# Optimization experiments

Hardware: AMD Instinct MI355X
Metric: run time of the kernel (lower is better)

## Reference

```python
import jax, jax.numpy as jnp
import numpy as np

B, N, D, H, L = 2, 2048, 512, 8, 2
HD = D // H


def setup_inputs() -> dict:
    key = jax.random.key(0)
    ks = jax.random.split(key, 8)
    s = 0.02
    return {
        "inputs_embeds": jax.random.normal(ks[0], (B, N, D), jnp.float32),
        "pos_emb": jax.random.normal(ks[1], (N, D), jnp.float32) * s,
        "c_attn_w": jax.random.normal(ks[2], (L, D, 3 * D), jnp.float32) * s,
        "c_attn_b": jnp.zeros((L, 3 * D), jnp.float32),
        "out_w": jax.random.normal(ks[3], (L, D, D), jnp.float32) * s,
        "out_b": jnp.zeros((L, D), jnp.float32),
        "ln1_g": jnp.ones((L, D), jnp.float32),
        "ln1_b": jnp.zeros((L, D), jnp.float32),
        "c_fc_w": jax.random.normal(ks[4], (L, D, 4 * D), jnp.float32) * s,
        "c_fc_b": jnp.zeros((L, 4 * D), jnp.float32),
        "c_proj_w": jax.random.normal(ks[5], (L, 4 * D, D), jnp.float32) * s,
        "c_proj_b": jnp.zeros((L, D), jnp.float32),
        "ln2_g": jnp.ones((L, D), jnp.float32),
        "ln2_b": jnp.zeros((L, D), jnp.float32),
    }


def _layernorm(x, g, b, eps=1e-5):
    mu = jnp.mean(x, axis=-1, keepdims=True)
    var = jnp.mean(jnp.square(x - mu), axis=-1, keepdims=True)
    return (x - mu) * jax.lax.rsqrt(var + eps) * g + b


def _gelu_new(x):
    # NewGELUActivation: tanh approximation
    return 0.5 * x * (1.0 + jnp.tanh(jnp.sqrt(2.0 / jnp.pi) * (x + 0.044715 * x ** 3)))


def _attention(x, w_qkv, b_qkv, w_out, b_out, self_mask):
    qkv = x @ w_qkv + b_qkv                      # [B,N,3D]
    q, k, v = jnp.split(qkv, 3, axis=-1)
    def heads(t):
        return t.reshape(B, N, H, HD).transpose(0, 2, 1, 3)  # [B,H,N,HD]
    q, k, v = heads(q), heads(k), heads(v)
    scores = jnp.einsum('bhqd,bhkd->bhqk', q, k) / jnp.sqrt(jnp.float32(HD))
    neg = jnp.finfo(scores.dtype).min
    scores = jnp.where(self_mask, scores, neg)   # exclude-self mask
    attn = jax.nn.softmax(scores, axis=-1)
    o = jnp.einsum('bhqk,bhkd->bhqd', attn, v)
    o = o.transpose(0, 2, 1, 3).reshape(B, N, D)
    return o @ w_out + b_out


def reference(inputs_embeds, pos_emb, c_attn_w, c_attn_b, out_w, out_b,
              ln1_g, ln1_b, c_fc_w, c_fc_b, c_proj_w, c_proj_b, ln2_g, ln2_b):
    self_mask = ~jnp.eye(N, dtype=bool)[None, None]  # [1,1,N,N]
    h = inputs_embeds + pos_emb[None]
    for l in range(L):
        res = h
        x = _layernorm(h, ln1_g[l], ln1_b[l])
        h = _attention(x, c_attn_w[l], c_attn_b[l], out_w[l], out_b[l], self_mask) + res
        res = h
        x = _layernorm(h, ln2_g[l], ln2_b[l])
        x = _gelu_new(x @ c_fc_w[l] + c_fc_b[l])
        h = (x @ c_proj_w[l] + c_proj_b[l]) + res
    return h
```

## Files before the change

kernel.cpp:

```cpp
#include <hip/hip_runtime.h>
#include <hip/hip_bf16.h>
#include <math.h>

#define BB 2
#define NN 2048
#define DD 512
#define HH 8
#define LL 2
#define TT (BB*NN)

typedef short short8 __attribute__((ext_vector_type(8)));
typedef float floatx4 __attribute__((ext_vector_type(4)));

__device__ __forceinline__ unsigned short f2b(float v) {
    union { float f; unsigned u; } x; x.f = v;
    unsigned r = x.u + 0x7fff + ((x.u >> 16) & 1);
    return (unsigned short)(r >> 16);
}

__global__ __launch_bounds__(256) void k_bias_add(const float* __restrict__ src,
                                                  const float* __restrict__ bias,
                                                  float* __restrict__ dst) {
    int i = blockIdx.x * 256 + threadIdx.x;
    dst[i] = src[i] + bias[i & (DD - 1)];
}

template <int EMB>
__global__ __launch_bounds__(256) void k_ln(const float* __restrict__ hin,
                                            unsigned short* __restrict__ xout,
                                            const float* __restrict__ g,
                                            const float* __restrict__ b,
                                            const float* __restrict__ emb,
                                            const float* __restrict__ pos,
                                            float* __restrict__ hout) {
    __shared__ float red[4];
    __shared__ float bc1, bc2;
    int t = blockIdx.x;
    int tid = threadIdx.x;
    int lane = tid & 63, wv = tid >> 6;
    float v0, v1;
    if (EMB) {
        const float* erow = emb + (size_t)t * DD;
        const float* prow = pos + (size_t)(t & (NN - 1)) * DD;
        v0 = erow[tid] + prow[tid];
        v1 = erow[tid + 256] + prow[tid + 256];
        hout[(size_t)t * DD + tid] = v0;
        hout[(size_t)t * DD + tid + 256] = v1;
    } else {
        const float* row = hin + (size_t)t * DD;
        v0 = row[tid];
        v1 = row[tid + 256];
    }

    float s = v0 + v1;
#pragma unroll
    for (int o = 32; o; o >>= 1) s += __shfl_down(s, o, 64);
    if (lane == 0) red[wv] = s;
    __syncthreads();
    if (tid == 0) bc1 = (red[0] + red[1] + red[2] + red[3]) * (1.0f / DD);
    __syncthreads();
    float mu = bc1;
    float d0 = v0 - mu, d1 = v1 - mu;
    s = d0 * d0 + d1 * d1;
#pragma unroll
    for (int o = 32; o; o >>= 1) s += __shfl_down(s, o, 64);
    if (lane == 0) red[wv] = s;
    __syncthreads();
    if (tid == 0) bc2 = (red[0] + red[1] + red[2] + red[3]) * (1.0f / DD);
    __syncthreads();
    float rstd = rsqrtf(bc2 + 1e-5f);
    xout[(size_t)t * DD + tid]       = f2b(d0 * rstd * g[tid] + b[tid]);
    xout[(size_t)t * DD + tid + 256] = f2b(d1 * rstd * g[tid + 256] + b[tid + 256]);
}

__device__ __forceinline__ float gelu_new(float v) {
    const float c = 0.7978845608028654f;
    float u = c * (v + 0.044715f * v * v * v);
    return 0.5f * v * (1.0f + tanhf(u));
}

#define PL 3145728
__global__ __launch_bounds__(256) void k_wt_all(const float* __restrict__ c_attn_w,
                                                const float* __restrict__ out_w,
                                                const float* __restrict__ c_fc_w,
                                                const float* __restrict__ c_proj_w,
                                                unsigned short* __restrict__ wbuf) {
    __shared__ unsigned short t[64][72];
    int bx = blockIdx.x;
    int l = bx / 768;
    int r = bx - l * 768;
    const float* W; unsigned short* WT; int K, N;
    if (r < 192)      { W = c_attn_w + (size_t)l * 512 * 1536; WT = wbuf + (size_t)l * PL;           K = 512;  N = 1536; }
    else if (r < 256) { r -= 192; W = out_w  + (size_t)l * 512 * 512;  WT = wbuf + (size_t)l * PL + 786432;  K = 512;  N = 512; }
    else if (r < 512) { r -= 256; W = c_fc_w + (size_t)l * 512 * 2048; WT = wbuf + (size_t)l * PL + 1048576; K = 512;  N = 2048; }
    else              { r -= 512; W = c_proj_w + (size_t)l * 2048 * 512; WT = wbuf + (size_t)l * PL + 2097152; K = 2048; N = 512; }
    int tiles_n = N >> 6;
    int n0 = (r % tiles_n) * 64, k0 = (r / tiles_n) * 64;

    int tid = threadIdx.x;
    int rr = tid >> 2;
    int c0 = (tid & 3) * 16;
    const float* src = W + (size_t)(k0 + rr) * N + n0 + c0;
#pragma unroll
    for (int u = 0; u < 4; u++) {
        float4 v = *(const float4*)&src[u * 4];
        t[c0 + u * 4 + 0][rr] = f2b(v.x);
        t[c0 + u * 4 + 1][rr] = f2b(v.y);
        t[c0 + u * 4 + 2][rr] = f2b(v.z);
        t[c0 + u * 4 + 3][rr] = f2b(v.w);
    }
    __syncthreads();
    unsigned short* dst = WT + (size_t)(n0 + rr) * K + k0 + c0;
#pragma unroll
    for (int u = 0; u < 4; u++)
        *(uint2*)&dst[u * 4] = *(const uint2*)&t[rr][c0 + u * 4];
}

template <int ACT, int BF16OUT, int ATOMIC>
__global__ __launch_bounds__(256) void k_mgemm(const unsigned short* __restrict__ Ab,
                                               const unsigned short* __restrict__ Bt,
                                               const float* __restrict__ bias,
                                               float* __restrict__ Cp,
                                               unsigned short* __restrict__ Cb,
                                               int Kfull, int Kchunk, int N) {
    __shared__ unsigned short Als[2][8 * 512];
    __shared__ unsigned short Bls[2][8 * 512];

    int tid = threadIdx.x;
    int l = tid & 63, w = tid >> 6;
    int wm = w >> 1, wn = w & 1;
    int m0 = blockIdx.y * 128, n0 = blockIdx.x * 128;
    int kb = blockIdx.z * Kchunk;
    int lr = l & 15;
    int lk = (l >> 4) * 8;

    const unsigned short* Ap0 = Ab + (size_t)(m0 + (w * 2 + 0) * 16 + lr) * Kfull + kb + lk;
    const unsigned short* Ap1 = Ab + (size_t)(m0 + (w * 2 + 1) * 16 + lr) * Kfull + kb + lk;
    const unsigned short* Bp0 = Bt + (size_t)(n0 + (w * 2 + 0) * 16 + lr) * Kfull + kb + lk;
    const unsigned short* Bp1 = Bt + (size_t)(n0 + (w * 2 + 1) * 16 + lr) * Kfull + kb + lk;
    int la0 = (w * 2 + 0) * 512 + l * 8;
    int la1 = (w * 2 + 1) * 512 + l * 8;

    floatx4 acc[4][4];
#pragma unroll
    for (int i = 0; i < 4; i++)
#pragma unroll
        for (int j = 0; j < 4; j++) acc[i][j] = (floatx4){0.f, 0.f, 0.f, 0.f};

    int nit = Kchunk >> 5;

    uint4 ra0 = *(const uint4*)Ap0;
    uint4 ra1 = *(const uint4*)Ap1;
    uint4 rb0 = *(const uint4*)Bp0;
    uint4 rb1 = *(const uint4*)Bp1;
    *(uint4*)&Als[0][la0] = ra0;
    *(uint4*)&Als[0][la1] = ra1;
    *(uint4*)&Bls[0][la0] = rb0;
    *(uint4*)&Bls[0][la1] = rb1;
    if (nit > 1) {
        ra0 = *(const uint4*)(Ap0 + 32);
        ra1 = *(const uint4*)(Ap1 + 32);
        rb0 = *(const uint4*)(Bp0 + 32);
        rb1 = *(const uint4*)(Bp1 + 32);
    }
    __syncthreads();

    for (int it = 0; it < nit; it++) {
        int c = it & 1;
        if (it + 1 < nit) {
            *(uint4*)&Als[c ^ 1][la0] = ra0;
            *(uint4*)&Als[c ^ 1][la1] = ra1;
            *(uint4*)&Bls[c ^ 1][la0] = rb0;
            *(uint4*)&Bls[c ^ 1][la1] = rb1;
        }
        if (it + 2 < nit) {
            int ko = (it + 2) << 5;
            ra0 = *(const uint4*)(Ap0 + ko);
            ra1 = *(const uint4*)(Ap1 + ko);
            rb0 = *(const uint4*)(Bp0 + ko);
            rb1 = *(const uint4*)(Bp1 + ko);
        }
        short8 a[4], b[4];
#pragma unroll
        for (int i = 0; i < 4; i++) {
            a[i] = *(const short8*)&Als[c][(wm * 4 + i) * 512 + l * 8];
            b[i] = *(const short8*)&Bls[c][(wn * 4 + i) * 512 + l * 8];
        }
#pragma unroll
        for (int i = 0; i < 4; i++)
#pragma unroll
            for (int j = 0; j < 4; j++)
                acc[i][j] = __builtin_amdgcn_mfma_f32_16x16x32_bf16(a[i], b[j], acc[i][j], 0, 0, 0);
        __syncthreads();
    }

    int col_in = l & 15, rquad = (l >> 4) * 4;
    bool addb = (!ATOMIC) || (bias != nullptr && blockIdx.z == 0);
#pragma unroll
    for (int i = 0; i < 4; i++) {
        int gm_base = m0 + wm * 64 + i * 16 + rquad;
#pragma unroll
        for (int j = 0; j < 4; j++) {
            int gn = n0 + wn * 64 + j * 16 + col_in;
            float bv = addb ? bias[gn] : 0.0f;
#pragma unroll
            for (int r = 0; r < 4; r++) {
                size_t off = (size_t)(gm_base + r) * N + gn;
                if (ATOMIC) {
                    atomicAdd(&Cp[off], acc[i][j][r] + bv);
                } else {
                    float v = acc[i][j][r] + bv;
                    if (ACT) v = gelu_new(v);
                    if (BF16OUT) Cb[off] = f2b(v);
                    else Cp[off] = v;
                }
            }
        }
    }
}

__global__ __launch_bounds__(256) void k_attn_mfma(const unsigned short* __restrict__ qkv,
                                                   unsigned short* __restrict__ xatt) {
    __shared__ unsigned short Ks[64 * 72];
    __shared__ unsigned short Vt[64 * 72];
    __shared__ unsigned short Pls[64 * 72];

    int qt = blockIdx.x, hd = blockIdx.y, b = blockIdx.z;
    int tid = threadIdx.x;
    int l = tid & 63, w = tid >> 6;
    int lr = l & 15, quad = l >> 4;

    const size_t base = (size_t)b * NN * 1536;

    short8 qf[2];
    {
        const unsigned short* qrow = qkv + base + (size_t)(qt * 64 + w * 16 + lr) * 1536 + hd * 64;
        qf[0] = *(const short8*)&qrow[quad * 8];
        qf[1] = *(const short8*)&qrow[quad * 8 + 32];
    }

    floatx4 O[4];
#pragma unroll
    for (int jd = 0; jd < 4; jd++) O[jd] = (floatx4){0.f, 0.f, 0.f, 0.f};
    float lsum = 0.0f;

    int sr = tid >> 2, sc = (tid & 3) * 16;
    int vk = (tid & 15) * 4, vd = (tid >> 4) * 4;
    const unsigned short* Kbase = qkv + base + 512 + hd * 64;
    const unsigned short* Vbase = qkv + base + 1024 + hd * 64;

    uint4 rk0, rk1;
    union { uint2 u; unsigned short s[4]; } rv[4];
    rk0 = *(const uint4*)&Kbase[(size_t)sr * 1536 + sc];
    rk1 = *(const uint4*)&Kbase[(size_t)sr * 1536 + sc + 8];
#pragma unroll
    for (int i = 0; i < 4; i++)
        rv[i].u = *(const uint2*)&Vbase[(size_t)(vk + i) * 1536 + vd];

    for (int kt = 0; kt < 32; kt++) {
        __syncthreads();
        *(uint4*)&Ks[sr * 72 + sc]     = rk0;
        *(uint4*)&Ks[sr * 72 + sc + 8] = rk1;
#pragma unroll
        for (int j = 0; j < 4; j++) {
            union { uint2 u; unsigned short s[4]; } pk;
            pk.s[0] = rv[0].s[j]; pk.s[1] = rv[1].s[j];
            pk.s[2] = rv[2].s[j]; pk.s[3] = rv[3].s[j];
            *(uint2*)&Vt[(vd + j) * 72 + vk] = pk.u;
        }
        __syncthreads();
        if (kt < 31) {
            int kn = (kt + 1) * 64;
            rk0 = *(const uint4*)&Kbase[(size_t)(kn + sr) * 1536 + sc];
            rk1 = *(const uint4*)&Kbase[(size_t)(kn + sr) * 1536 + sc + 8];
#pragma unroll
            for (int i = 0; i < 4; i++)
                rv[i].u = *(const uint2*)&Vbase[(size_t)(kn + vk + i) * 1536 + vd];
        }

        floatx4 s[4];
#pragma unroll
        for (int jn = 0; jn < 4; jn++) s[jn] = (floatx4){0.f, 0.f, 0.f, 0.f};
#pragma unroll
        for (int ss = 0; ss < 2; ss++)
#pragma unroll
            for (int jn = 0; jn < 4; jn++) {
                short8 ak = *(const short8*)&Ks[(jn * 16 + lr) * 72 + ss * 32 + quad * 8];
                s[jn] = __builtin_amdgcn_mfma_f32_16x16x32_bf16(ak, qf[ss], s[jn], 0, 0, 0);
            }

        int mq = w * 16 + lr;
#pragma unroll
        for (int jn = 0; jn < 4; jn++) {
            union { uint2 u; unsigned short h[4]; } pk;
#pragma unroll
            for (int r = 0; r < 4; r++) {
                float p = __expf(s[jn][r] * 0.125f - 8.0f);
                if (kt == qt && mq == jn * 16 + quad * 4 + r) p = 0.0f;
                lsum += p;
                pk.h[r] = f2b(p);
            }
            *(uint2*)&Pls[mq * 72 + jn * 16 + quad * 4] = pk.u;
        }

#pragma unroll
        for (int ss = 0; ss < 2; ss++) {
            short8 ap = *(const short8*)&Pls[(w * 16 + lr) * 72 + ss * 32 + quad * 8];
#pragma unroll
            for (int jd = 0; jd < 4; jd++) {
                short8 bv = *(const short8*)&Vt[(jd * 16 + lr) * 72 + ss * 32 + quad * 8];
                O[jd] = __builtin_amdgcn_mfma_f32_16x16x32_bf16(ap, bv, O[jd], 0, 0, 0);
            }
        }
    }

    lsum += __shfl_xor(lsum, 16);
    lsum += __shfl_xor(lsum, 32);
#pragma unroll
    for (int r = 0; r < 4; r++) {
        float inv = 1.0f / __shfl(lsum, quad * 4 + r, 16);
        size_t tok = (size_t)b * NN + qt * 64 + w * 16 + quad * 4 + r;
#pragma unroll
        for (int jd = 0; jd < 4; jd++)
            xatt[tok * DD + hd * 64 + jd * 16 + lr] = f2b(O[jd][r] * inv);
    }
}

extern "C" void kernel_launch(void* const* d_in, const int* in_sizes, int n_in,
                              void* d_out, int out_size, void* d_ws, size_t ws_size,
                              hipStream_t stream) {
    const float* emb      = (const float*)d_in[0];
    const float* pos      = (const float*)d_in[1];
    const float* c_attn_w = (const float*)d_in[2];
    const float* c_attn_b = (const float*)d_in[3];
    const float* out_w    = (const float*)d_in[4];
    const float* out_b    = (const float*)d_in[5];
    const float* ln1_g    = (const float*)d_in[6];
    const float* ln1_b    = (const float*)d_in[7];
    const float* c_fc_w   = (const float*)d_in[8];
    const float* c_fc_b   = (const float*)d_in[9];
    const float* c_proj_w = (const float*)d_in[10];
    const float* c_proj_b = (const float*)d_in[11];
    const float* ln2_g    = (const float*)d_in[12];
    const float* ln2_b    = (const float*)d_in[13];

    char* p = (char*)d_ws;
    float* h = (float*)p;                       p += (size_t)TT * DD * 4;
    unsigned short* act = (unsigned short*)p;   p += (size_t)TT * 2048 * 2;
    unsigned short* x = (unsigned short*)p;     p += (size_t)TT * DD * 2;
    unsigned short* xatt = (unsigned short*)p;  p += (size_t)TT * DD * 2;
    unsigned short* wbuf = (unsigned short*)p;

    unsigned short* qkvb = act;
    unsigned short* ffa  = act;
    float* out = (float*)d_out;

    k_wt_all<<<1536, 256, 0, stream>>>(c_attn_w, out_w, c_fc_w, c_proj_w, wbuf);

    for (int l = 0; l < LL; l++) {
        unsigned short* wqkv_t  = wbuf + (size_t)l * PL;
        unsigned short* wout_t  = wqkv_t + 786432;
        unsigned short* wfc_t   = wqkv_t + 1048576;
        unsigned short* wproj_t = wqkv_t + 2097152;

        if (l == 0)
            k_ln<1><<<TT, 256, 0, stream>>>(nullptr, x, ln1_g, ln1_b, emb, pos, h);
        else
            k_ln<0><<<TT, 256, 0, stream>>>(h, x, ln1_g + l * DD, ln1_b + l * DD,
                                            nullptr, nullptr, nullptr);
        k_mgemm<0, 1, 0><<<dim3(1536 / 128, TT / 128), 256, 0, stream>>>(
            x, wqkv_t, c_attn_b + l * 1536, nullptr, qkvb, 512, 512, 1536);
        k_attn_mfma<<<dim3(NN / 64, HH, BB), 256, 0, stream>>>(qkvb, xatt);
        k_mgemm<0, 0, 1><<<dim3(512 / 128, TT / 128, 2), 256, 0, stream>>>(
            xatt, wout_t, out_b + l * DD, h, nullptr, 512, 256, 512);
        k_ln<0><<<TT, 256, 0, stream>>>(h, x, ln2_g + l * DD, ln2_b + l * DD,
                                        nullptr, nullptr, nullptr);
        k_mgemm<1, 1, 0><<<dim3(2048 / 128, TT / 128), 256, 0, stream>>>(
            x, wfc_t, c_fc_b + l * 2048, nullptr, ffa, 512, 512, 2048);
        if (l == LL - 1) {
            k_bias_add<<<TT * DD / 256, 256, 0, stream>>>(h, c_proj_b + l * DD, out);
            k_mgemm<0, 0, 1><<<dim3(512 / 128, TT / 128, 4), 256, 0, stream>>>(
                ffa, wproj_t, nullptr, out, nullptr, 2048, 512, 512);
        } else {
            k_mgemm<0, 0, 1><<<dim3(512 / 128, TT / 128, 4), 256, 0, stream>>>(
                ffa, wproj_t, c_proj_b + l * DD, h, nullptr, 2048, 512, 512);
        }
    }
}
```

Measured before the change: 432.5 us.

## Split attention KV range across two blocks and combine partial outputs

The attention kernel's key/value loop is split in two halves, each handled by a separate block, which doubles the grid along z. Each half writes unnormalized partial outputs in bf16 plus per-row partial softmax sums. A new elementwise kernel adds the two partials and normalizes. The aim is better occupancy and latency hiding, since the original grid had only about two blocks per CU. The cost is an extra launch, extra memory traffic for the partials, and bf16 rounding of the unnormalized partials.

```diff
diff --git a/kernel.cpp b/kernel.cpp
--- a/kernel.cpp
+++ b/kernel.cpp
@@ -16,6 +16,10 @@
     union { float f; unsigned u; } x; x.f = v;
     unsigned r = x.u + 0x7fff + ((x.u >> 16) & 1);
     return (unsigned short)(r >> 16);
+}
+
+__device__ __forceinline__ float b2f(unsigned short b) {
+    union { unsigned u; float f; } x; x.u = ((unsigned)b) << 16; return x.f;
 }
 
 __global__ __launch_bounds__(256) void k_bias_add(const float* __restrict__ src,
@@ -220,12 +224,19 @@
 }
 
 __global__ __launch_bounds__(256) void k_attn_mfma(const unsigned short* __restrict__ qkv,
-                                                   unsigned short* __restrict__ xatt) {
+                                                   unsigned short* __restrict__ op0,
+                                                   unsigned short* __restrict__ op1,
+                                                   float* __restrict__ lsump) {
     __shared__ unsigned short Ks[64 * 72];
     __shared__ unsigned short Vt[64 * 72];
     __shared__ unsigned short Pls[64 * 72];
 
-    int qt = blockIdx.x, hd = blockIdx.y, b = blockIdx.z;
+    int qt = blockIdx.x, hd = blockIdx.y;
+    int z = blockIdx.z;
+    int b = z >> 1, half = z & 1;
+    int kt0 = half * 16, kt1 = kt0 + 16;
+    unsigned short* dst = half ? op1 : op0;
+
     int tid = threadIdx.x;
     int l = tid & 63, w = tid >> 6;
     int lr = l & 15, quad = l >> 4;
@@ -251,13 +262,14 @@
 
     uint4 rk0, rk1;
     union { uint2 u; unsigned short s[4]; } rv[4];
-    rk0 = *(const uint4*)&Kbase[(size_t)sr * 1536 + sc];
-    rk1 = *(const uint4*)&Kbase[(size_t)sr * 1536 + sc + 8];
+    int kb0 = kt0 * 64;
+    rk0 = *(const uint4*)&Kbase[(size_t)(kb0 + sr) * 1536 + sc];
+    rk1 = *(const uint4*)&Kbase[(size_t)(kb0 + sr) * 1536 + sc + 8];
 #pragma unroll
     for (int i = 0; i < 4; i++)
-        rv[i].u = *(const uint2*)&Vbase[(size_t)(vk + i) * 1536 + vd];
-
-    for (int kt = 0; kt < 32; kt++) {
+        rv[i].u = *(const uint2*)&Vbase[(size_t)(kb0 + vk + i) * 1536 + vd];
+
+    for (int kt = kt0; kt < kt1; kt++) {
         __syncthreads();
         *(uint4*)&Ks[sr * 72 + sc]     = rk0;
         *(uint4*)&Ks[sr * 72 + sc + 8] = rk1;
@@ -269,7 +281,7 @@
             *(uint2*)&Vt[(vd + j) * 72 + vk] = pk.u;
         }
         __syncthreads();
-        if (kt < 31) {
+        if (kt < kt1 - 1) {
             int kn = (kt + 1) * 64;
             rk0 = *(const uint4*)&Kbase[(size_t)(kn + sr) * 1536 + sc];
             rk1 = *(const uint4*)&Kbase[(size_t)(kn + sr) * 1536 + sc + 8];
@@ -316,14 +328,33 @@
 
     lsum += __shfl_xor(lsum, 16);
     lsum += __shfl_xor(lsum, 32);
+    if (quad == 0)
+        lsump[(size_t)(half * TT + b * NN + qt * 64 + w * 16 + lr) * HH + hd] = lsum;
+
 #pragma unroll
     for (int r = 0; r < 4; r++) {
-        float inv = 1.0f / __shfl(lsum, quad * 4 + r, 16);
         size_t tok = (size_t)b * NN + qt * 64 + w * 16 + quad * 4 + r;
 #pragma unroll
         for (int jd = 0; jd < 4; jd++)
-            xatt[tok * DD + hd * 64 + jd * 16 + lr] = f2b(O[jd][r] * inv);
-    }
+            dst[tok * DD + hd * 64 + jd * 16 + lr] = f2b(O[jd][r]);
+    }
+}
+
+__global__ __launch_bounds__(256) void k_attn_comb(const unsigned short* __restrict__ op0,
+                                                   unsigned short* __restrict__ xatt,
+                                                   const float* __restrict__ lsump) {
+    int i = (blockIdx.x * 256 + threadIdx.x) * 4;
+    int tok = i >> 9;
+    int hd = (i & 511) >> 6;
+    float inv = 1.0f / (lsump[(size_t)tok * HH + hd] +
+                        lsump[(size_t)(TT + tok) * HH + hd]);
+    union { uint2 u; unsigned short s[4]; } a0, a1, o;
+    a0.u = *(const uint2*)&op0[i];
+    a1.u = *(const uint2*)&xatt[i];
+#pragma unroll
+    for (int u = 0; u < 4; u++)
+        o.s[u] = f2b((b2f(a0.s[u]) + b2f(a1.s[u])) * inv);
+    *(uint2*)&xatt[i] = o.u;
 }
 
 extern "C" void kernel_launch(void* const* d_in, const int* in_sizes, int n_in,
@@ -349,9 +380,11 @@
     unsigned short* act = (unsigned short*)p;   p += (size_t)TT * 2048 * 2;
     unsigned short* x = (unsigned short*)p;     p += (size_t)TT * DD * 2;
     unsigned short* xatt = (unsigned short*)p;  p += (size_t)TT * DD * 2;
-    unsigned short* wbuf = (unsigned short*)p;
+    unsigned short* wbuf = (unsigned short*)p;  p += (size_t)2 * PL * 2;
+    float* lsump = (float*)p;
 
     unsigned short* qkvb = act;
+    unsigned short* opart0 = act + (size_t)TT * 1536;
     unsigned short* ffa  = act;
     float* out = (float*)d_out;
 
@@ -370,7 +403,8 @@
                                             nullptr, nullptr, nullptr);
         k_mgemm<0, 1, 0><<<dim3(1536 / 128, TT / 128), 256, 0, stream>>>(
             x, wqkv_t, c_attn_b + l * 1536, nullptr, qkvb, 512, 512, 1536);
-        k_attn_mfma<<<dim3(NN / 64, HH, BB), 256, 0, stream>>>(qkvb, xatt);
+        k_attn_mfma<<<dim3(NN / 64, HH, BB * 2), 256, 0, stream>>>(qkvb, opart0, xatt, lsump);
+        k_attn_comb<<<TT * DD / 1024, 256, 0, stream>>>(opart0, xatt, lsump);
         k_mgemm<0, 0, 1><<<dim3(512 / 128, TT / 128, 2), 256, 0, stream>>>(
             xatt, wout_t, out_b + l * DD, h, nullptr, 512, 256, 512);
         k_ln<0><<<TT, 256, 0, stream>>>(h, x, ln2_g + l * DD, ln2_b + l * DD,
```

Result: no change. 433.0 us (+0.1%).
